# Kernel tuning notes

Measured on AMD Instinct MI355X. Metric: run time of the kernel, lower is better.

## Reference

```python
import jax, jax.numpy as jnp
import numpy as np

N, K, F = 8192, 64, 128  # nodes, neighbors (nb_sparse), feature map width


def setup_inputs() -> dict:
    key = jax.random.key(0)
    k1, k2, k3, k4 = jax.random.split(key, 4)
    return {
        "emb_in": jax.random.normal(k1, (N, F), dtype=jnp.float32),
        "sum_weights": jax.random.uniform(k2, (N,), dtype=jnp.float32),
        "idx_in": jax.random.randint(k3, (N, K - 1), 0, N),  # neighbor indices (KNN output)
        "edge_out": jax.random.normal(k4, (N, K), dtype=jnp.float32),  # edge-net output, resized to [N, K]
    }


def reference(emb_in, sum_weights, idx_in, edge_out):
    n, f = emb_in.shape
    k = idx_in.shape[1] + 1
    # append self-index as the last neighbor (as in make_samples)
    idx = jnp.concatenate([idx_in, jnp.arange(n, dtype=idx_in.dtype)[:, None]], axis=1)  # [N, K]

    # --- make_samples: gather-concat, fully vectorized over nodes ---
    node = jnp.broadcast_to(emb_in[:, None, :], (n, k, f))          # node repeated k times
    neighbors = emb_in[idx]                                          # [N, K, F] gather
    edge_wts = sum_weights[idx][..., None]                           # [N, K, 1]
    samples = jnp.concatenate([node, neighbors, edge_wts], axis=-1).reshape(n * k, 2 * f + 1)

    # --- get_adj: sequential row build; `line` carries over between rows (faithful to torch code) ---
    def step(line, xs):
        idx_i, e_i = xs
        line = line.at[idx_i].set(e_i)
        return line, line

    line0 = jnp.zeros((n,), dtype=edge_out.dtype)
    _, adj = jax.lax.scan(step, line0, (idx, edge_out))  # adj: [N, N]

    return samples, adj
```

## Files before the change

### kernel.cpp

```cpp
#include <hip/hip_runtime.h>
#include <cstdint>

#define N_NODES 8192
#define K_NB    64
#define F_DIM   128
#define SAMP_W  (2 * F_DIM + 1)
#define ROWS_PER_BLK 64
#define NBLK (N_NODES / ROWS_PER_BLK)
#define CW   2048
#define NCHUNK (N_NODES / CW)

static __device__ __forceinline__ unsigned long long pack_uv(unsigned int ord, float v) {
    return ((unsigned long long)ord << 32) | (unsigned long long)__float_as_uint(v);
}
static __device__ __forceinline__ float unpack_v(unsigned long long p) {
    return __uint_as_float((unsigned int)(p & 0xffffffffULL));
}

__global__ __launch_bounds__(256) void samples_kernel(
    const float* __restrict__ emb, const float* __restrict__ sw,
    const int* __restrict__ idx, float* __restrict__ out)
{
    const int i = blockIdx.x;
    const int t = threadIdx.x;
    float nd = 0.0f;
    if (t < F_DIM) nd = emb[i * F_DIM + t];
    const int rowbase = i * (K_NB * SAMP_W);
    for (int j = 0; j < K_NB; ++j) {
        const int c = (j < K_NB - 1) ? idx[i * (K_NB - 1) + j] : i;
        const int base = rowbase + j * SAMP_W;
        if (t < F_DIM) {
            out[base + t] = nd;
            if (t == 0) out[base + 2 * F_DIM] = sw[c];
        } else {
            out[base + t] = emb[c * F_DIM + (t - F_DIM)];
        }
    }
}

__global__ __launch_bounds__(256) void p1_kernel(
    const int* __restrict__ idx, const float* __restrict__ edge,
    unsigned long long* __restrict__ S)
{
    __shared__ unsigned long long line[N_NODES];
    const int b = blockIdx.x;
    const int t = threadIdx.x;
    for (int k = t; k < N_NODES; k += 256) line[k] = 0ULL;
    __syncthreads();
    for (int u = t; u < ROWS_PER_BLK * K_NB; u += 256) {
        const int r = b * ROWS_PER_BLK + (u >> 6);
        const int j = u & 63;
        const int c = (j < K_NB - 1) ? idx[r * (K_NB - 1) + j] : r;
        const float v = edge[r * K_NB + j];
        atomicMax(&line[c], pack_uv((unsigned)(r * K_NB + j + 1), v));
    }
    __syncthreads();
    for (int k = t; k < N_NODES; k += 256) S[b * N_NODES + k] = line[k];
}

__global__ __launch_bounds__(256) void p2_kernel(
    const unsigned long long* __restrict__ S, float* __restrict__ carry)
{
    const int c = blockIdx.x * 256 + threadIdx.x;
    unsigned long long run = 0ULL;
    for (int b = 0; b < NBLK; ++b) {
        carry[b * N_NODES + c] = unpack_v(run);
        const unsigned long long s = S[b * N_NODES + c];
        if (s != 0ULL) run = s;
    }
}

__global__ __launch_bounds__(256) void p3_kernel(
    const int* __restrict__ idx, const float* __restrict__ edge,
    const float* __restrict__ carry, float* __restrict__ adj)
{
    __shared__ unsigned long long line[CW];
    const int b  = blockIdx.x;
    const int c0 = blockIdx.y * CW;
    const int t  = threadIdx.x;
    for (int k = t; k < CW; k += 256)
        line[k] = pack_uv(0u, carry[b * N_NODES + c0 + k]);
    __syncthreads();
    for (int rr = 0; rr < ROWS_PER_BLK; ++rr) {
        const int r = b * ROWS_PER_BLK + rr;
        if (t < K_NB) {
            const int j = t;
            const int c = (j < K_NB - 1) ? idx[r * (K_NB - 1) + j] : r;
            const unsigned int cc = (unsigned)(c - c0);
            if (cc < (unsigned)CW) {
                const float v = edge[r * K_NB + j];
                atomicMax(&line[cc], pack_uv((unsigned)(r * K_NB + j + 1), v));
            }
        }
        __syncthreads();
        const int rowbase = r * N_NODES + c0;
        for (int k = t; k < CW; k += 256)
            adj[rowbase + k] = unpack_v(line[k]);
        __syncthreads();
    }
}

extern "C" void kernel_launch(void* const* d_in, const int* in_sizes, int n_in,
                              void* d_out, int out_size, void* d_ws, size_t ws_size,
                              hipStream_t stream)
{
    const float* emb  = (const float*)d_in[0];
    const float* sw   = (const float*)d_in[1];
    const int*   idx  = (const int*)d_in[2];
    const float* edge = (const float*)d_in[3];

    float* out      = (float*)d_out;
    float* samples  = out;
    float* adj      = out + (size_t)N_NODES * K_NB * SAMP_W;

    unsigned long long* S = (unsigned long long*)d_out;
    float* carry = (float*)((char*)d_out + (size_t)NBLK * N_NODES * 8);

    p1_kernel<<<NBLK, 256, 0, stream>>>(idx, edge, S);
    p2_kernel<<<N_NODES / 256, 256, 0, stream>>>(S, carry);
    p3_kernel<<<dim3(NBLK, NCHUNK), 256, 0, stream>>>(idx, edge, carry, adj);
    samples_kernel<<<N_NODES, 256, 0, stream>>>(emb, sw, idx, samples);
}
```

Baseline: 1.006 ms.

## Vectorize samples and adjacency stores, shrink chunk width, retune scan launch

The samples kernel now assigns one wave per neighbor row and moves data as float4 loads and stores instead of scalar per-thread copies. In the adjacency kernel the chunk width is halved so each thread owns four contiguous columns, and rows are written out with float4 stores from 16-byte shared reads. The carry scan kernel moves to 64-thread blocks with an unrolled loop. Barriers are replaced by explicit waitcnt plus s_barrier. Together these aim to cut store instruction count and raise memory throughput, at the cost of twice as many p3 blocks re-reading idx and edge, and unaligned float4 stores into the 257-wide sample rows.

```diff
diff --git a/kernel.cpp b/kernel.cpp
--- a/kernel.cpp
+++ b/kernel.cpp
@@ -7,7 +7,7 @@
 #define SAMP_W  (2 * F_DIM + 1)
 #define ROWS_PER_BLK 64
 #define NBLK (N_NODES / ROWS_PER_BLK)
-#define CW   2048
+#define CW   1024
 #define NCHUNK (N_NODES / CW)
 
 static __device__ __forceinline__ unsigned long long pack_uv(unsigned int ord, float v) {
@@ -22,19 +22,20 @@
     const int* __restrict__ idx, float* __restrict__ out)
 {
     const int i = blockIdx.x;
-    const int t = threadIdx.x;
-    float nd = 0.0f;
-    if (t < F_DIM) nd = emb[i * F_DIM + t];
-    const int rowbase = i * (K_NB * SAMP_W);
-    for (int j = 0; j < K_NB; ++j) {
+    const int w = threadIdx.x >> 6;
+    const int l = threadIdx.x & 63;
+    float4 nd4 = make_float4(0.f, 0.f, 0.f, 0.f);
+    if (l < 32) nd4 = *reinterpret_cast<const float4*>(&emb[i * F_DIM + 4 * l]);
+    #pragma unroll 4
+    for (int j = w; j < K_NB; j += 4) {
         const int c = (j < K_NB - 1) ? idx[i * (K_NB - 1) + j] : i;
-        const int base = rowbase + j * SAMP_W;
-        if (t < F_DIM) {
-            out[base + t] = nd;
-            if (t == 0) out[base + 2 * F_DIM] = sw[c];
-        } else {
-            out[base + t] = emb[c * F_DIM + (t - F_DIM)];
-        }
+        const float swc = sw[c];
+        float4 v;
+        if (l < 32) v = nd4;
+        else        v = *reinterpret_cast<const float4*>(&emb[c * F_DIM + 4 * (l - 32)]);
+        const size_t base = (size_t)(i * K_NB + j) * SAMP_W;
+        __builtin_memcpy(out + base + 4 * l, &v, sizeof(float4));
+        if (l == 0) out[base + 2 * F_DIM] = swc;
     }
 }
 
@@ -58,11 +59,12 @@
     for (int k = t; k < N_NODES; k += 256) S[b * N_NODES + k] = line[k];
 }
 
-__global__ __launch_bounds__(256) void p2_kernel(
+__global__ __launch_bounds__(64) void p2_kernel(
     const unsigned long long* __restrict__ S, float* __restrict__ carry)
 {
-    const int c = blockIdx.x * 256 + threadIdx.x;
+    const int c = blockIdx.x * 64 + threadIdx.x;
     unsigned long long run = 0ULL;
+    #pragma unroll 8
     for (int b = 0; b < NBLK; ++b) {
         carry[b * N_NODES + c] = unpack_v(run);
         const unsigned long long s = S[b * N_NODES + c];
@@ -74,29 +76,43 @@
     const int* __restrict__ idx, const float* __restrict__ edge,
     const float* __restrict__ carry, float* __restrict__ adj)
 {
-    __shared__ unsigned long long line[CW];
+    __shared__ alignas(16) unsigned long long line[CW];
     const int b  = blockIdx.x;
     const int c0 = blockIdx.y * CW;
     const int t  = threadIdx.x;
-    for (int k = t; k < CW; k += 256)
-        line[k] = pack_uv(0u, carry[b * N_NODES + c0 + k]);
-    __syncthreads();
+    const int k4 = t * 4;
+
+    {
+        const float4 cv = *reinterpret_cast<const float4*>(&carry[(size_t)b * N_NODES + c0 + k4]);
+        line[k4 + 0] = pack_uv(0u, cv.x);
+        line[k4 + 1] = pack_uv(0u, cv.y);
+        line[k4 + 2] = pack_uv(0u, cv.z);
+        line[k4 + 3] = pack_uv(0u, cv.w);
+    }
+    asm volatile("s_waitcnt lgkmcnt(0)" ::: "memory");
+    __builtin_amdgcn_s_barrier();
+
     for (int rr = 0; rr < ROWS_PER_BLK; ++rr) {
         const int r = b * ROWS_PER_BLK + rr;
         if (t < K_NB) {
-            const int j = t;
-            const int c = (j < K_NB - 1) ? idx[r * (K_NB - 1) + j] : r;
-            const unsigned int cc = (unsigned)(c - c0);
+            const int c = (t < K_NB - 1) ? idx[r * (K_NB - 1) + t] : r;
+            const unsigned cc = (unsigned)(c - c0);
             if (cc < (unsigned)CW) {
-                const float v = edge[r * K_NB + j];
-                atomicMax(&line[cc], pack_uv((unsigned)(r * K_NB + j + 1), v));
+                atomicMax(&line[cc], pack_uv((unsigned)(r * K_NB + t + 1), edge[r * K_NB + t]));
             }
         }
-        __syncthreads();
-        const int rowbase = r * N_NODES + c0;
-        for (int k = t; k < CW; k += 256)
-            adj[rowbase + k] = unpack_v(line[k]);
-        __syncthreads();
+        asm volatile("s_waitcnt lgkmcnt(0)" ::: "memory");
+        __builtin_amdgcn_s_barrier();
+
+        const ulonglong2 p0 = *reinterpret_cast<const ulonglong2*>(&line[k4]);
+        const ulonglong2 p1 = *reinterpret_cast<const ulonglong2*>(&line[k4 + 2]);
+        float4 v;
+        v.x = unpack_v(p0.x); v.y = unpack_v(p0.y);
+        v.z = unpack_v(p1.x); v.w = unpack_v(p1.y);
+        *reinterpret_cast<float4*>(&adj[(size_t)r * N_NODES + c0 + k4]) = v;
+
+        asm volatile("s_waitcnt lgkmcnt(0)" ::: "memory");
+        __builtin_amdgcn_s_barrier();
     }
 }
 
@@ -117,7 +133,7 @@
     float* carry = (float*)((char*)d_out + (size_t)NBLK * N_NODES * 8);
 
     p1_kernel<<<NBLK, 256, 0, stream>>>(idx, edge, S);
-    p2_kernel<<<N_NODES / 256, 256, 0, stream>>>(S, carry);
+    p2_kernel<<<N_NODES / 64, 64, 0, stream>>>(S, carry);
     p3_kernel<<<dim3(NBLK, NCHUNK), 256, 0, stream>>>(idx, edge, carry, adj);
     samples_kernel<<<N_NODES, 256, 0, stream>>>(emb, sw, idx, samples);
 }
```

Measured after the change: 880.4 us. 1.14x faster.
